# Optimization experiments

Hardware: AMD Instinct MI355X
Metric: run time of the kernel (lower is better)

The kernel has to match this reference:

```python
import jax, jax.numpy as jnp
import numpy as np

N_NODES = 100000   # nodes per node type
N_EDGES = 800000   # edges per edge type
F_IN = 128         # lazy (-1,-1) input feature dim, chosen == hidden
HID = 128          # hidden_channels
OUT = 1            # out_channels
N_LAYERS = 2
B = 256            # batch_size (num graphs)
NEG_SLOPE = 0.2    # GATConv default leaky_relu slope


def setup_inputs() -> dict:
    key = jax.random.key(0)
    ks = jax.random.split(key, 16)
    x_i = jax.random.normal(ks[0], (N_NODES, F_IN), jnp.float32)
    x_j = jax.random.normal(ks[1], (N_NODES, F_IN), jnp.float32)
    ei_ii = jax.random.randint(ks[2], (2, N_EDGES), 0, N_NODES, jnp.int32)
    ei_jj = jax.random.randint(ks[3], (2, N_EDGES), 0, N_NODES, jnp.int32)
    ei_ij = jax.random.randint(ks[4], (2, N_EDGES), 0, N_NODES, jnp.int32)
    ei_ji = jax.random.randint(ks[5], (2, N_EDGES), 0, N_NODES, jnp.int32)
    batch_i = jnp.sort(jax.random.randint(ks[6], (N_NODES,), 0, B, jnp.int32))
    batch_j = jnp.sort(jax.random.randint(ks[7], (N_NODES,), 0, B, jnp.int32))
    s = 1.0 / np.sqrt(HID)
    Ws = jax.random.normal(ks[8], (N_LAYERS, 4, F_IN, HID), jnp.float32) * s
    Wd = jax.random.normal(ks[9], (N_LAYERS, 4, F_IN, HID), jnp.float32) * s
    att_s = jax.random.normal(ks[10], (N_LAYERS, 4, HID), jnp.float32) * s
    att_d = jax.random.normal(ks[11], (N_LAYERS, 4, HID), jnp.float32) * s
    bias = jnp.zeros((N_LAYERS, 4, HID), jnp.float32)
    lin_w = jax.random.normal(ks[12], (HID, OUT), jnp.float32) * s
    lin_b = jnp.zeros((OUT,), jnp.float32)
    return dict(x_i=x_i, x_j=x_j, ei_ii=ei_ii, ei_jj=ei_jj, ei_ij=ei_ij,
                ei_ji=ei_ji, batch_i=batch_i, batch_j=batch_j, Ws=Ws, Wd=Wd,
                att_s=att_s, att_d=att_d, bias=bias, lin_w=lin_w, lin_b=lin_b)


def gat_conv(x_src, x_dst, edge, W_s, W_d, a_s, a_d, b):
    """Single-head GATConv: gather -> edge attention -> segment softmax -> scatter."""
    src, dst = edge[0], edge[1]
    n_dst = x_dst.shape[0]
    hs = x_src @ W_s                      # [Ns, C]
    hd = x_dst @ W_d                      # [Nd, C]
    e = jax.nn.leaky_relu((hs * a_s).sum(-1)[src] + (hd * a_d).sum(-1)[dst],
                          NEG_SLOPE)      # [E]
    m = jax.ops.segment_max(e, dst, num_segments=n_dst)
    m = jnp.where(jnp.isfinite(m), m, 0.0)  # empty segments -> 0
    p = jnp.exp(e - m[dst])
    denom = jax.ops.segment_sum(p, dst, num_segments=n_dst)
    alpha = p / jnp.maximum(denom[dst], 1e-16)
    out = jax.ops.segment_sum(alpha[:, None] * hs[src], dst, num_segments=n_dst)
    return out + b


def mean_pool(x, batch, size):
    s = jax.ops.segment_sum(x, batch, num_segments=size)
    cnt = jax.ops.segment_sum(jnp.ones((x.shape[0],), x.dtype), batch,
                              num_segments=size)
    return s / jnp.maximum(cnt, 1.0)[:, None]


def reference(x_i, x_j, ei_ii, ei_jj, ei_ij, ei_ji, batch_i, batch_j,
              Ws, Wd, att_s, att_d, bias, lin_w, lin_b):
    xi, xj = x_i, x_j
    for l in range(N_LAYERS):
        # edge-type order: 0=inner_i, 1=inner_j, 2=outer_ij, 3=outer_ji
        out_i = (gat_conv(xi, xi, ei_ii, Ws[l, 0], Wd[l, 0], att_s[l, 0], att_d[l, 0], bias[l, 0])
                 + gat_conv(xj, xi, ei_ji, Ws[l, 3], Wd[l, 3], att_s[l, 3], att_d[l, 3], bias[l, 3]))
        out_j = (gat_conv(xj, xj, ei_jj, Ws[l, 1], Wd[l, 1], att_s[l, 1], att_d[l, 1], bias[l, 1])
                 + gat_conv(xi, xj, ei_ij, Ws[l, 2], Wd[l, 2], att_s[l, 2], att_d[l, 2], bias[l, 2]))
        xi, xj = jnp.tanh(out_i), jnp.tanh(out_j)
    p_i = mean_pool(xi, batch_i, B)       # [B, HID]
    p_j = mean_pool(xj, batch_j, B)       # [B, HID]
    x = 0.5 * (p_i + p_j)                 # mean over the stacked pair
    return jax.nn.sigmoid(x @ lin_w + lin_b)
```

## Files before the change

### kernel.cpp

```cpp
#include <hip/hip_runtime.h>


#define NEG_SLOPE 0.2f

typedef __attribute__((ext_vector_type(8))) short short8v;
typedef __attribute__((ext_vector_type(4))) float float4v;

__device__ __forceinline__ unsigned short f2bf(float f) {
  unsigned u = __float_as_uint(f);
  unsigned r = (u + 0x7FFFu + ((u >> 16) & 1u)) >> 16;
  return (unsigned short)r;
}
__device__ __forceinline__ unsigned pack2(float a, float b) {
  return (unsigned)f2bf(a) | ((unsigned)f2bf(b) << 16);
}
__device__ __forceinline__ float bflo(unsigned u) {
  return __uint_as_float(u << 16);
}
__device__ __forceinline__ float bfhi(unsigned u) {
  return __uint_as_float(u & 0xFFFF0000u);
}
__device__ __forceinline__ float rl_f(float x, int lane) {
  return __int_as_float(__builtin_amdgcn_readlane(__float_as_int(x), lane));
}
__device__ __forceinline__ int rl_i(int x, int lane) {
  return __builtin_amdgcn_readlane(x, lane);
}

__global__ __launch_bounds__(256) void w_to_bf16t(const float* __restrict__ W,
                                                  unsigned short* __restrict__ Wt) {
  __shared__ float buf[64][129];
  int b = blockIdx.x, t = threadIdx.x;
  const float* w = W + (size_t)b * 16384;
  unsigned short* o = Wt + (size_t)b * 16384;
  for (int h = 0; h < 2; ++h) {
    for (int i = 0; i < 32; ++i) {
      int idx = i * 256 + t;
      buf[idx >> 7][idx & 127] = w[(size_t)(h * 64 + (idx >> 7)) * 128 + (idx & 127)];
    }
    __syncthreads();
    for (int i = 0; i < 32; ++i) {
      int idx = i * 256 + t;
      o[(size_t)(idx >> 6) * 128 + h * 64 + (idx & 63)] = f2bf(buf[idx & 63][idx >> 6]);
    }
    __syncthreads();
  }
}

__global__ void precompute_wa(const float* __restrict__ W,
                              const float* __restrict__ att,
                              float* __restrict__ out) {
  int idx = blockIdx.x;
  int f = threadIdx.x;
  const float* w = W + (size_t)idx * 128 * 128 + (size_t)f * 128;
  const float* a = att + idx * 128;
  float s = 0.f;
  #pragma unroll 8
  for (int h = 0; h < 128; ++h) s += w[h] * a[h];
  out[idx * 128 + f] = s;
}

template <int XBF16>
__global__ __launch_bounds__(256) void gemm_dual(
    const void* __restrict__ Xv,
    const unsigned short* __restrict__ Wt1, const float* __restrict__ att1,
    unsigned short* __restrict__ Hb1, float* __restrict__ as1,
    const unsigned short* __restrict__ Wt2, const float* __restrict__ att2,
    unsigned short* __restrict__ Hb2, float* __restrict__ as2,
    const float* __restrict__ vdA, const float* __restrict__ vdB,
    float* __restrict__ adA, float* __restrict__ adB, int M) {
  __shared__ unsigned short Xt[64][136];
  __shared__ unsigned short Wt[128][136];
  const int t = threadIdx.x;
  const int row0 = blockIdx.x * 64;

  {
    int r = t >> 2;
    int cq = (t & 3) * 32;
    int gr = row0 + r;
    if (gr >= M) gr = M - 1;
    if (XBF16) {
      const unsigned short* Xb = (const unsigned short*)Xv;
      const uint4* src = (const uint4*)(Xb + (size_t)gr * 128 + cq);
      #pragma unroll
      for (int i = 0; i < 4; ++i) *(uint4*)&Xt[r][cq + i * 8] = src[i];
    } else {
      const float* Xf = (const float*)Xv;
      const float4* src = (const float4*)(Xf + (size_t)gr * 128 + cq);
      #pragma unroll
      for (int i = 0; i < 8; ++i) {
        float4 v = src[i];
        uint2 u;
        u.x = pack2(v.x, v.y);
        u.y = pack2(v.z, v.w);
        *(uint2*)&Xt[r][cq + i * 4] = u;
      }
    }
  }
  {
    int n = t >> 1;
    int kh = (t & 1) * 64;
    const uint4* src = (const uint4*)(Wt1 + (size_t)n * 128 + kh);
    #pragma unroll
    for (int i = 0; i < 8; ++i) *(uint4*)&Wt[n][kh + i * 8] = src[i];
  }
  __syncthreads();

  if (t < 128) {
    int r = t & 63;
    const float* vd = (t < 64) ? vdA : vdB;
    float* adout = (t < 64) ? adA : adB;
    float sum = 0.f;
    #pragma unroll 4
    for (int k8 = 0; k8 < 16; ++k8) {
      uint4 u = *(const uint4*)&Xt[r][k8 * 8];
      const float* v = vd + k8 * 8;
      sum = fmaf(bflo(u.x), v[0], sum);
      sum = fmaf(bfhi(u.x), v[1], sum);
      sum = fmaf(bflo(u.y), v[2], sum);
      sum = fmaf(bfhi(u.y), v[3], sum);
      sum = fmaf(bflo(u.z), v[4], sum);
      sum = fmaf(bfhi(u.z), v[5], sum);
      sum = fmaf(bflo(u.w), v[6], sum);
      sum = fmaf(bfhi(u.w), v[7], sum);
    }
    int gr = row0 + r;
    if (gr < M) adout[gr] = sum;
  }

  const int lane = t & 63;
  const int wv = t >> 6;
  const int m = lane & 15;
  const int g = lane >> 4;
  const int ws = wv * 16;

  for (int ww = 0; ww < 2; ++ww) {
    if (ww == 1) {
      __syncthreads();
      int n = t >> 1;
      int kh = (t & 1) * 64;
      const uint4* src = (const uint4*)(Wt2 + (size_t)n * 128 + kh);
      #pragma unroll
      for (int i = 0; i < 8; ++i) *(uint4*)&Wt[n][kh + i * 8] = src[i];
      __syncthreads();
    }
    const float* att = ww ? att2 : att1;
    unsigned short* Hb = ww ? Hb2 : Hb1;
    float* as_ = ww ? as2 : as1;

    float4v acc[8];
    float4v z = {0.f, 0.f, 0.f, 0.f};
    #pragma unroll
    for (int nt = 0; nt < 8; ++nt) acc[nt] = z;

    #pragma unroll
    for (int ks = 0; ks < 4; ++ks) {
      short8v a = *(const short8v*)&Xt[ws + m][ks * 32 + g * 8];
      #pragma unroll
      for (int nt = 0; nt < 8; ++nt) {
        short8v b = *(const short8v*)&Wt[nt * 16 + m][ks * 32 + g * 8];
        acc[nt] = __builtin_amdgcn_mfma_f32_16x16x32_bf16(a, b, acc[nt], 0, 0, 0);
      }
    }

    {
      float attv[8];
      #pragma unroll
      for (int nt = 0; nt < 8; ++nt) attv[nt] = att[nt * 16 + m];
      #pragma unroll
      for (int r = 0; r < 4; ++r) {
        float s = 0.f;
        #pragma unroll
        for (int nt = 0; nt < 8; ++nt) s = fmaf(acc[nt][r], attv[nt], s);
        #pragma unroll
        for (int off = 1; off < 16; off <<= 1) s += __shfl_xor(s, off);
        if (m == 0) {
          int grow = row0 + ws + g * 4 + r;
          if (grow < M) as_[grow] = s;
        }
      }
    }

    #pragma unroll
    for (int nt = 0; nt < 8; ++nt) {
      #pragma unroll
      for (int r = 0; r < 4; ++r) {
        float v = acc[nt][r];
        float vn = __shfl_xor(v, 1);
        if ((m & 1) == 0) {
          int grow = row0 + ws + g * 4 + r;
          if (grow < M) {
            *(unsigned*)(Hb + (size_t)grow * 128 + nt * 16 + m) = pack2(v, vn);
          }
        }
      }
    }
  }
}

__global__ void hist4(const int* __restrict__ e0, const int* __restrict__ e1,
                      const int* __restrict__ e2, const int* __restrict__ e3,
                      int E, int* __restrict__ deg, int N) {
  int i = blockIdx.x * 256 + threadIdx.x;
  if (i >= E) return;
  int t = blockIdx.y;
  const int* ei = (t == 0) ? e0 : (t == 1) ? e1 : (t == 2) ? e2 : e3;
  atomicAdd(&deg[t * N + ei[E + i]], 1);
}

__global__ __launch_bounds__(1024) void scan4(const int* __restrict__ deg,
                                              int* __restrict__ rowptr, int N) {
  __shared__ int sums[1024];
  int t = threadIdx.x;
  int ty = blockIdx.x;
  const int* d = deg + (size_t)ty * N;
  int* rp = rowptr + (size_t)ty * (N + 1);
  int chunk = (N + 1023) / 1024;
  int lo = t * chunk;
  int hi = lo + chunk; if (hi > N) hi = N; if (lo > N) lo = N;
  int s = 0;
  for (int i = lo; i < hi; ++i) s += d[i];
  sums[t] = s;
  __syncthreads();
  for (int off = 1; off < 1024; off <<= 1) {
    int add = (t >= off) ? sums[t - off] : 0;
    __syncthreads();
    sums[t] += add;
    __syncthreads();
  }
  int run = (t == 0) ? 0 : sums[t - 1];
  for (int i = lo; i < hi; ++i) {
    rp[i] = run;
    run += d[i];
  }
  if (t == 1023) rp[N] = sums[1023];
}

__global__ void fill4(const int* __restrict__ e0, const int* __restrict__ e1,
                      const int* __restrict__ e2, const int* __restrict__ e3,
                      int E, const int* __restrict__ rowptr,
                      int* __restrict__ fill, int* __restrict__ csrc, int N) {
  int i = blockIdx.x * 256 + threadIdx.x;
  if (i >= E) return;
  int t = blockIdx.y;
  const int* ei = (t == 0) ? e0 : (t == 1) ? e1 : (t == 2) ? e2 : e3;
  int d = ei[E + i];
  int s = ei[i];
  int pos = rowptr[(size_t)t * (N + 1) + d] + atomicAdd(&fill[t * N + d], 1);
  csrc[(size_t)t * E + pos] = s;
}

__device__ __forceinline__ float2 agg_conv(const int* __restrict__ rowptr,
                                           const int* __restrict__ csrc,
                                           const unsigned short* __restrict__ hs,
                                           const float* __restrict__ as_,
                                           float ad, int n, int lane) {
  int beg = rowptr[n], end = rowptr[n + 1];
  float lsum = 0.f;
  float2 acc = make_float2(0.f, 0.f);
  for (int c = beg; c < end; c += 64) {
    int k = c + lane;
    bool valid = k < end;
    int s = valid ? csrc[k] : 0;
    float e = valid ? (as_[s] + ad) : 0.f;
    e = e > 0.f ? e : NEG_SLOPE * e;
    float p = valid ? __expf(e) : 0.f;
    float ps = p;
    #pragma unroll
    for (int off = 32; off >= 1; off >>= 1) ps += __shfl_xor(ps, off);
    lsum += ps;
    int cnt = end - c; if (cnt > 64) cnt = 64;
    for (int base = 0; base < cnt; base += 8) {
      float pk0 = rl_f(p, base + 0), pk1 = rl_f(p, base + 1);
      float pk2 = rl_f(p, base + 2), pk3 = rl_f(p, base + 3);
      float pk4 = rl_f(p, base + 4), pk5 = rl_f(p, base + 5);
      float pk6 = rl_f(p, base + 6), pk7 = rl_f(p, base + 7);
      int sk0 = rl_i(s, base + 0), sk1 = rl_i(s, base + 1);
      int sk2 = rl_i(s, base + 2), sk3 = rl_i(s, base + 3);
      int sk4 = rl_i(s, base + 4), sk5 = rl_i(s, base + 5);
      int sk6 = rl_i(s, base + 6), sk7 = rl_i(s, base + 7);
      unsigned u0 = *(const unsigned*)(hs + (size_t)sk0 * 128 + lane * 2);
      unsigned u1 = *(const unsigned*)(hs + (size_t)sk1 * 128 + lane * 2);
      unsigned u2 = *(const unsigned*)(hs + (size_t)sk2 * 128 + lane * 2);
      unsigned u3 = *(const unsigned*)(hs + (size_t)sk3 * 128 + lane * 2);
      unsigned u4 = *(const unsigned*)(hs + (size_t)sk4 * 128 + lane * 2);
      unsigned u5 = *(const unsigned*)(hs + (size_t)sk5 * 128 + lane * 2);
      unsigned u6 = *(const unsigned*)(hs + (size_t)sk6 * 128 + lane * 2);
      unsigned u7 = *(const unsigned*)(hs + (size_t)sk7 * 128 + lane * 2);
      acc.x = fmaf(pk0, bflo(u0), acc.x); acc.y = fmaf(pk0, bfhi(u0), acc.y);
      acc.x = fmaf(pk1, bflo(u1), acc.x); acc.y = fmaf(pk1, bfhi(u1), acc.y);
      acc.x = fmaf(pk2, bflo(u2), acc.x); acc.y = fmaf(pk2, bfhi(u2), acc.y);
      acc.x = fmaf(pk3, bflo(u3), acc.x); acc.y = fmaf(pk3, bfhi(u3), acc.y);
      acc.x = fmaf(pk4, bflo(u4), acc.x); acc.y = fmaf(pk4, bfhi(u4), acc.y);
      acc.x = fmaf(pk5, bflo(u5), acc.x); acc.y = fmaf(pk5, bfhi(u5), acc.y);
      acc.x = fmaf(pk6, bflo(u6), acc.x); acc.y = fmaf(pk6, bfhi(u6), acc.y);
      acc.x = fmaf(pk7, bflo(u7), acc.x); acc.y = fmaf(pk7, bfhi(u7), acc.y);
    }
  }
  float inv = 1.f / fmaxf(lsum, 1e-16f);
  acc.x *= inv;
  acc.y *= inv;
  return acc;
}

__global__ __launch_bounds__(256) void fused_agg_store(
    const int* __restrict__ rA, const int* __restrict__ sA,
    const unsigned short* __restrict__ hA, const float* __restrict__ asA,
    const float* __restrict__ adA, const int* __restrict__ rB,
    const int* __restrict__ sB, const unsigned short* __restrict__ hB,
    const float* __restrict__ asB, const float* __restrict__ adB,
    const float* __restrict__ biasA, const float* __restrict__ biasB,
    unsigned short* __restrict__ out, int N) {
  int wave = (blockIdx.x * 256 + threadIdx.x) >> 6;
  int lane = threadIdx.x & 63;
  if (wave >= N) return;
  float2 a = agg_conv(rA, sA, hA, asA, adA[wave], wave, lane);
  float2 b = agg_conv(rB, sB, hB, asB, adB[wave], wave, lane);
  float2 b1 = *(const float2*)(biasA + lane * 2);
  float2 b2 = *(const float2*)(biasB + lane * 2);
  float vx = tanhf(a.x + b.x + b1.x + b2.x);
  float vy = tanhf(a.y + b.y + b1.y + b2.y);
  *(unsigned*)(out + (size_t)wave * 128 + lane * 2) = pack2(vx, vy);
}

__global__ __launch_bounds__(256) void fused_agg_pool(
    const int* __restrict__ rA, const int* __restrict__ sA,
    const unsigned short* __restrict__ hA, const float* __restrict__ asA,
    const float* __restrict__ adA, const int* __restrict__ rB,
    const int* __restrict__ sB, const unsigned short* __restrict__ hB,
    const float* __restrict__ asB, const float* __restrict__ adB,
    const float* __restrict__ biasA, const float* __restrict__ biasB,
    const int* __restrict__ batch, float* __restrict__ pool, int N) {
  int wave = (blockIdx.x * 256 + threadIdx.x) >> 6;
  int lane = threadIdx.x & 63;
  if (wave >= N) return;
  float2 a = agg_conv(rA, sA, hA, asA, adA[wave], wave, lane);
  float2 b = agg_conv(rB, sB, hB, asB, adB[wave], wave, lane);
  float2 b1 = *(const float2*)(biasA + lane * 2);
  float2 b2 = *(const float2*)(biasB + lane * 2);
  float vx = tanhf(a.x + b.x + b1.x + b2.x);
  float vy = tanhf(a.y + b.y + b1.y + b2.y);
  int bb = batch[wave];
  float* p = pool + (size_t)bb * 128 + lane * 2;
  unsafeAtomicAdd(p, vx);
  unsafeAtomicAdd(p + 1, vy);
}

__device__ __forceinline__ int lower_bound_i(const int* __restrict__ a, int n,
                                             int v) {
  int lo = 0, hi = n;
  while (lo < hi) {
    int mid = (lo + hi) >> 1;
    if (a[mid] < v) lo = mid + 1; else hi = mid;
  }
  return lo;
}

__global__ void final_k(const float* __restrict__ pool_i,
                        const int* __restrict__ batch_i,
                        const float* __restrict__ pool_j,
                        const int* __restrict__ batch_j, int N,
                        const float* __restrict__ lin_w,
                        const float* __restrict__ lin_b,
                        float* __restrict__ out) {
  int b = threadIdx.x;
  float ci = (float)(lower_bound_i(batch_i, N, b + 1) -
                     lower_bound_i(batch_i, N, b));
  float cj = (float)(lower_bound_i(batch_j, N, b + 1) -
                     lower_bound_i(batch_j, N, b));
  ci = fmaxf(ci, 1.f);
  cj = fmaxf(cj, 1.f);
  float acc = 0.f;
  #pragma unroll 4
  for (int f = 0; f < 128; ++f) {
    float x = 0.5f * (pool_i[(size_t)b * 128 + f] / ci +
                      pool_j[(size_t)b * 128 + f] / cj);
    acc += x * lin_w[f];
  }
  acc += lin_b[0];
  out[b] = 1.f / (1.f + __expf(-acc));
}

extern "C" void kernel_launch(void* const* d_in, const int* in_sizes, int n_in,
                              void* d_out, int out_size, void* d_ws,
                              size_t ws_size, hipStream_t stream) {
  const float* x_i = (const float*)d_in[0];
  const float* x_j = (const float*)d_in[1];
  const int* ei_arr[4] = {(const int*)d_in[2], (const int*)d_in[3],
                          (const int*)d_in[4], (const int*)d_in[5]};
  const int* batch_i = (const int*)d_in[6];
  const int* batch_j = (const int*)d_in[7];
  const float* Ws = (const float*)d_in[8];
  const float* Wd = (const float*)d_in[9];
  const float* att_s = (const float*)d_in[10];
  const float* att_d = (const float*)d_in[11];
  const float* bias = (const float*)d_in[12];
  const float* lin_w = (const float*)d_in[13];
  const float* lin_b = (const float*)d_in[14];
  float* out = (float*)d_out;

  const int N = in_sizes[0] / 128;
  const int E = in_sizes[2] / 2;
  const size_t NF = (size_t)N * 128;

  char* w = (char*)d_ws;
  auto alloc = [&](size_t bytes) {
    char* p = w;
    w += (bytes + 255) & ~(size_t)255;
    return p;
  };
  unsigned short* bufA_i = (unsigned short*)alloc(NF * 2);
  unsigned short* bufA_j = (unsigned short*)alloc(NF * 2);
  unsigned short* hsb[4];
  for (int c = 0; c < 4; ++c) hsb[c] = (unsigned short*)alloc(NF * 2);
  int* csrc = (int*)alloc((size_t)4 * E * 4);
  int* rowptr = (int*)alloc((size_t)4 * (N + 1) * 4);
  int* deg = (int*)alloc((size_t)4 * N * 4);
  int* fillc = (int*)alloc((size_t)4 * N * 4);
  float* asb[4];
  for (int c = 0; c < 4; ++c) asb[c] = (float*)alloc((size_t)N * 4);
  float* adb[4];
  for (int c = 0; c < 4; ++c) adb[c] = (float*)alloc((size_t)N * 4);
  float* wdad = (float*)alloc(8 * 128 * 4);
  unsigned short* Wst = (unsigned short*)alloc(8 * 16384 * 2);
  float* pool = (float*)alloc(2 * 256 * 128 * 4);
  float* pool_i = pool;
  float* pool_j = pool + 256 * 128;

  w_to_bf16t<<<8, 256, 0, stream>>>(Ws, Wst);
  precompute_wa<<<8, 128, 0, stream>>>(Wd, att_d, wdad);

  hipMemsetAsync(deg, 0, (size_t)4 * N * 4, stream);
  hipMemsetAsync(fillc, 0, (size_t)4 * N * 4, stream);
  dim3 egrid((E + 255) / 256, 4);
  hist4<<<egrid, 256, 0, stream>>>(ei_arr[0], ei_arr[1], ei_arr[2], ei_arr[3],
                                   E, deg, N);
  scan4<<<4, 1024, 0, stream>>>(deg, rowptr, N);
  fill4<<<egrid, 256, 0, stream>>>(ei_arr[0], ei_arr[1], ei_arr[2], ei_arr[3],
                                   E, rowptr, fillc, csrc, N);

  hipMemsetAsync(pool, 0, 2 * 256 * 128 * 4, stream);

  const int gemm_blocks = (N + 63) / 64;
  const int nodew_blocks = (N + 3) / 4;

  for (int l = 0; l < 2; ++l) {
    const void* cur_i = (l == 0) ? (const void*)x_i : (const void*)bufA_i;
    const void* cur_j = (l == 0) ? (const void*)x_j : (const void*)bufA_j;
    const size_t L = (size_t)l * 4;

    if (l == 0) {
      gemm_dual<0><<<gemm_blocks, 256, 0, stream>>>(
          cur_i, Wst + (L + 0) * 16384, att_s + (L + 0) * 128, hsb[0], asb[0],
          Wst + (L + 2) * 16384, att_s + (L + 2) * 128, hsb[2], asb[2],
          wdad + (L + 0) * 128, wdad + (L + 3) * 128, adb[0], adb[3], N);
      gemm_dual<0><<<gemm_blocks, 256, 0, stream>>>(
          cur_j, Wst + (L + 1) * 16384, att_s + (L + 1) * 128, hsb[1], asb[1],
          Wst + (L + 3) * 16384, att_s + (L + 3) * 128, hsb[3], asb[3],
          wdad + (L + 1) * 128, wdad + (L + 2) * 128, adb[1], adb[2], N);
    } else {
      gemm_dual<1><<<gemm_blocks, 256, 0, stream>>>(
          cur_i, Wst + (L + 0) * 16384, att_s + (L + 0) * 128, hsb[0], asb[0],
          Wst + (L + 2) * 16384, att_s + (L + 2) * 128, hsb[2], asb[2],
          wdad + (L + 0) * 128, wdad + (L + 3) * 128, adb[0], adb[3], N);
      gemm_dual<1><<<gemm_blocks, 256, 0, stream>>>(
          cur_j, Wst + (L + 1) * 16384, att_s + (L + 1) * 128, hsb[1], asb[1],
          Wst + (L + 3) * 16384, att_s + (L + 3) * 128, hsb[3], asb[3],
          wdad + (L + 1) * 128, wdad + (L + 2) * 128, adb[1], adb[2], N);
    }

    for (int pair = 0; pair < 2; ++pair) {
      int cA = (pair == 0) ? 0 : 1;
      int cB = (pair == 0) ? 3 : 2;
      const int* rA = rowptr + (size_t)cA * (N + 1);
      const int* rB = rowptr + (size_t)cB * (N + 1);
      const int* sA = csrc + (size_t)cA * E;
      const int* sB = csrc + (size_t)cB * E;
      const float* bA = bias + (L + cA) * 128;
      const float* bB = bias + (L + cB) * 128;
      if (l == 0) {
        unsigned short* outb = (pair == 0) ? bufA_i : bufA_j;
        fused_agg_store<<<nodew_blocks, 256, 0, stream>>>(
            rA, sA, hsb[cA], asb[cA], adb[cA], rB, sB, hsb[cB], asb[cB],
            adb[cB], bA, bB, outb, N);
      } else {
        const int* batch = (pair == 0) ? batch_i : batch_j;
        float* poolp = (pair == 0) ? pool_i : pool_j;
        fused_agg_pool<<<nodew_blocks, 256, 0, stream>>>(
            rA, sA, hsb[cA], asb[cA], adb[cA], rB, sB, hsb[cB], asb[cB],
            adb[cB], bA, bB, batch, poolp, N);
      }
    }
  }

  final_k<<<1, 256, 0, stream>>>(pool_i, batch_i, pool_j, batch_j, N, lin_w,
                                 lin_b, out);
}
```

Before: 1.179 ms.

## Interleave both edge types' gathers per node and merge pair launches into one grid

The per-node aggregation now walks both incoming edge types in the same loop, issuing 16 independent feature-row gathers per step instead of 8, to expose more memory-level parallelism. The softmax denominator is accumulated from readlane values rather than a separate wave shuffle reduction. The two per-destination-type launches are merged into a single 2D grid, which removes a launch and the tail between them. In exchange, register pressure rises and when degrees differ the loop runs to the larger of the two counts, with some lanes doing masked work.

```diff
diff --git a/kernel.cpp b/kernel.cpp
--- a/kernel.cpp
+++ b/kernel.cpp
@@ -250,94 +250,129 @@
   csrc[(size_t)t * E + pos] = s;
 }
 
-__device__ __forceinline__ float2 agg_conv(const int* __restrict__ rowptr,
-                                           const int* __restrict__ csrc,
-                                           const unsigned short* __restrict__ hs,
-                                           const float* __restrict__ as_,
-                                           float ad, int n, int lane) {
-  int beg = rowptr[n], end = rowptr[n + 1];
-  float lsum = 0.f;
-  float2 acc = make_float2(0.f, 0.f);
-  for (int c = beg; c < end; c += 64) {
-    int k = c + lane;
-    bool valid = k < end;
-    int s = valid ? csrc[k] : 0;
-    float e = valid ? (as_[s] + ad) : 0.f;
-    e = e > 0.f ? e : NEG_SLOPE * e;
-    float p = valid ? __expf(e) : 0.f;
-    float ps = p;
-    #pragma unroll
-    for (int off = 32; off >= 1; off >>= 1) ps += __shfl_xor(ps, off);
-    lsum += ps;
-    int cnt = end - c; if (cnt > 64) cnt = 64;
+struct PairArgs {
+  const int* rA; const int* sA; const unsigned short* hA;
+  const float* asA; const float* adA;
+  const int* rB; const int* sB; const unsigned short* hB;
+  const float* asB; const float* adB;
+  const float* biasA; const float* biasB;
+};
+
+__device__ __forceinline__ void agg_pair(const PairArgs& P, int n, int lane,
+                                         float2& outA, float2& outB) {
+  int begA = P.rA[n], endA = P.rA[n + 1];
+  int begB = P.rB[n], endB = P.rB[n + 1];
+  float adA = P.adA[n], adB = P.adB[n];
+  float lsA = 0.f, lsB = 0.f;
+  float2 aA = make_float2(0.f, 0.f), aB = make_float2(0.f, 0.f);
+  int cA = begA, cB = begB;
+  while (cA < endA || cB < endB) {
+    int kA = cA + lane, kB = cB + lane;
+    bool vA = kA < endA;
+    bool vB = kB < endB;
+    int sA = vA ? P.sA[kA] : 0;
+    int sB = vB ? P.sB[kB] : 0;
+    float eA = vA ? (P.asA[sA] + adA) : 0.f;
+    float eB = vB ? (P.asB[sB] + adB) : 0.f;
+    eA = eA > 0.f ? eA : NEG_SLOPE * eA;
+    eB = eB > 0.f ? eB : NEG_SLOPE * eB;
+    float pA = vA ? __expf(eA) : 0.f;
+    float pB = vB ? __expf(eB) : 0.f;
+    int cntA = endA - cA; cntA = cntA < 0 ? 0 : (cntA > 64 ? 64 : cntA);
+    int cntB = endB - cB; cntB = cntB < 0 ? 0 : (cntB > 64 ? 64 : cntB);
+    int cnt = cntA > cntB ? cntA : cntB;
     for (int base = 0; base < cnt; base += 8) {
-      float pk0 = rl_f(p, base + 0), pk1 = rl_f(p, base + 1);
-      float pk2 = rl_f(p, base + 2), pk3 = rl_f(p, base + 3);
-      float pk4 = rl_f(p, base + 4), pk5 = rl_f(p, base + 5);
-      float pk6 = rl_f(p, base + 6), pk7 = rl_f(p, base + 7);
-      int sk0 = rl_i(s, base + 0), sk1 = rl_i(s, base + 1);
-      int sk2 = rl_i(s, base + 2), sk3 = rl_i(s, base + 3);
-      int sk4 = rl_i(s, base + 4), sk5 = rl_i(s, base + 5);
-      int sk6 = rl_i(s, base + 6), sk7 = rl_i(s, base + 7);
-      unsigned u0 = *(const unsigned*)(hs + (size_t)sk0 * 128 + lane * 2);
-      unsigned u1 = *(const unsigned*)(hs + (size_t)sk1 * 128 + lane * 2);
-      unsigned u2 = *(const unsigned*)(hs + (size_t)sk2 * 128 + lane * 2);
-      unsigned u3 = *(const unsigned*)(hs + (size_t)sk3 * 128 + lane * 2);
-      unsigned u4 = *(const unsigned*)(hs + (size_t)sk4 * 128 + lane * 2);
-      unsigned u5 = *(const unsigned*)(hs + (size_t)sk5 * 128 + lane * 2);
-      unsigned u6 = *(const unsigned*)(hs + (size_t)sk6 * 128 + lane * 2);
-      unsigned u7 = *(const unsigned*)(hs + (size_t)sk7 * 128 + lane * 2);
-      acc.x = fmaf(pk0, bflo(u0), acc.x); acc.y = fmaf(pk0, bfhi(u0), acc.y);
-      acc.x = fmaf(pk1, bflo(u1), acc.x); acc.y = fmaf(pk1, bfhi(u1), acc.y);
-      acc.x = fmaf(pk2, bflo(u2), acc.x); acc.y = fmaf(pk2, bfhi(u2), acc.y);
-      acc.x = fmaf(pk3, bflo(u3), acc.x); acc.y = fmaf(pk3, bfhi(u3), acc.y);
-      acc.x = fmaf(pk4, bflo(u4), acc.x); acc.y = fmaf(pk4, bfhi(u4), acc.y);
-      acc.x = fmaf(pk5, bflo(u5), acc.x); acc.y = fmaf(pk5, bfhi(u5), acc.y);
-      acc.x = fmaf(pk6, bflo(u6), acc.x); acc.y = fmaf(pk6, bfhi(u6), acc.y);
-      acc.x = fmaf(pk7, bflo(u7), acc.x); acc.y = fmaf(pk7, bfhi(u7), acc.y);
-    }
-  }
-  float inv = 1.f / fmaxf(lsum, 1e-16f);
-  acc.x *= inv;
-  acc.y *= inv;
-  return acc;
-}
-
-__global__ __launch_bounds__(256) void fused_agg_store(
-    const int* __restrict__ rA, const int* __restrict__ sA,
-    const unsigned short* __restrict__ hA, const float* __restrict__ asA,
-    const float* __restrict__ adA, const int* __restrict__ rB,
-    const int* __restrict__ sB, const unsigned short* __restrict__ hB,
-    const float* __restrict__ asB, const float* __restrict__ adB,
-    const float* __restrict__ biasA, const float* __restrict__ biasB,
-    unsigned short* __restrict__ out, int N) {
+      float qa0 = rl_f(pA, base + 0), qa1 = rl_f(pA, base + 1);
+      float qa2 = rl_f(pA, base + 2), qa3 = rl_f(pA, base + 3);
+      float qa4 = rl_f(pA, base + 4), qa5 = rl_f(pA, base + 5);
+      float qa6 = rl_f(pA, base + 6), qa7 = rl_f(pA, base + 7);
+      float qb0 = rl_f(pB, base + 0), qb1 = rl_f(pB, base + 1);
+      float qb2 = rl_f(pB, base + 2), qb3 = rl_f(pB, base + 3);
+      float qb4 = rl_f(pB, base + 4), qb5 = rl_f(pB, base + 5);
+      float qb6 = rl_f(pB, base + 6), qb7 = rl_f(pB, base + 7);
+      int ta0 = rl_i(sA, base + 0), ta1 = rl_i(sA, base + 1);
+      int ta2 = rl_i(sA, base + 2), ta3 = rl_i(sA, base + 3);
+      int ta4 = rl_i(sA, base + 4), ta5 = rl_i(sA, base + 5);
+      int ta6 = rl_i(sA, base + 6), ta7 = rl_i(sA, base + 7);
+      int tb0 = rl_i(sB, base + 0), tb1 = rl_i(sB, base + 1);
+      int tb2 = rl_i(sB, base + 2), tb3 = rl_i(sB, base + 3);
+      int tb4 = rl_i(sB, base + 4), tb5 = rl_i(sB, base + 5);
+      int tb6 = rl_i(sB, base + 6), tb7 = rl_i(sB, base + 7);
+      unsigned ua0 = *(const unsigned*)(P.hA + (size_t)ta0 * 128 + lane * 2);
+      unsigned ua1 = *(const unsigned*)(P.hA + (size_t)ta1 * 128 + lane * 2);
+      unsigned ua2 = *(const unsigned*)(P.hA + (size_t)ta2 * 128 + lane * 2);
+      unsigned ua3 = *(const unsigned*)(P.hA + (size_t)ta3 * 128 + lane * 2);
+      unsigned ua4 = *(const unsigned*)(P.hA + (size_t)ta4 * 128 + lane * 2);
+      unsigned ua5 = *(const unsigned*)(P.hA + (size_t)ta5 * 128 + lane * 2);
+      unsigned ua6 = *(const unsigned*)(P.hA + (size_t)ta6 * 128 + lane * 2);
+      unsigned ua7 = *(const unsigned*)(P.hA + (size_t)ta7 * 128 + lane * 2);
+      unsigned ub0 = *(const unsigned*)(P.hB + (size_t)tb0 * 128 + lane * 2);
+      unsigned ub1 = *(const unsigned*)(P.hB + (size_t)tb1 * 128 + lane * 2);
+      unsigned ub2 = *(const unsigned*)(P.hB + (size_t)tb2 * 128 + lane * 2);
+      unsigned ub3 = *(const unsigned*)(P.hB + (size_t)tb3 * 128 + lane * 2);
+      unsigned ub4 = *(const unsigned*)(P.hB + (size_t)tb4 * 128 + lane * 2);
+      unsigned ub5 = *(const unsigned*)(P.hB + (size_t)tb5 * 128 + lane * 2);
+      unsigned ub6 = *(const unsigned*)(P.hB + (size_t)tb6 * 128 + lane * 2);
+      unsigned ub7 = *(const unsigned*)(P.hB + (size_t)tb7 * 128 + lane * 2);
+      lsA += ((qa0 + qa1) + (qa2 + qa3)) + ((qa4 + qa5) + (qa6 + qa7));
+      lsB += ((qb0 + qb1) + (qb2 + qb3)) + ((qb4 + qb5) + (qb6 + qb7));
+      aA.x = fmaf(qa0, bflo(ua0), aA.x); aA.y = fmaf(qa0, bfhi(ua0), aA.y);
+      aA.x = fmaf(qa1, bflo(ua1), aA.x); aA.y = fmaf(qa1, bfhi(ua1), aA.y);
+      aA.x = fmaf(qa2, bflo(ua2), aA.x); aA.y = fmaf(qa2, bfhi(ua2), aA.y);
+      aA.x = fmaf(qa3, bflo(ua3), aA.x); aA.y = fmaf(qa3, bfhi(ua3), aA.y);
+      aA.x = fmaf(qa4, bflo(ua4), aA.x); aA.y = fmaf(qa4, bfhi(ua4), aA.y);
+      aA.x = fmaf(qa5, bflo(ua5), aA.x); aA.y = fmaf(qa5, bfhi(ua5), aA.y);
+      aA.x = fmaf(qa6, bflo(ua6), aA.x); aA.y = fmaf(qa6, bfhi(ua6), aA.y);
+      aA.x = fmaf(qa7, bflo(ua7), aA.x); aA.y = fmaf(qa7, bfhi(ua7), aA.y);
+      aB.x = fmaf(qb0, bflo(ub0), aB.x); aB.y = fmaf(qb0, bfhi(ub0), aB.y);
+      aB.x = fmaf(qb1, bflo(ub1), aB.x); aB.y = fmaf(qb1, bfhi(ub1), aB.y);
+      aB.x = fmaf(qb2, bflo(ub2), aB.x); aB.y = fmaf(qb2, bfhi(ub2), aB.y);
+      aB.x = fmaf(qb3, bflo(ub3), aB.x); aB.y = fmaf(qb3, bfhi(ub3), aB.y);
+      aB.x = fmaf(qb4, bflo(ub4), aB.x); aB.y = fmaf(qb4, bfhi(ub4), aB.y);
+      aB.x = fmaf(qb5, bflo(ub5), aB.x); aB.y = fmaf(qb5, bfhi(ub5), aB.y);
+      aB.x = fmaf(qb6, bflo(ub6), aB.x); aB.y = fmaf(qb6, bfhi(ub6), aB.y);
+      aB.x = fmaf(qb7, bflo(ub7), aB.x); aB.y = fmaf(qb7, bfhi(ub7), aB.y);
+    }
+    cA += 64;
+    cB += 64;
+  }
+  float invA = 1.f / fmaxf(lsA, 1e-16f);
+  float invB = 1.f / fmaxf(lsB, 1e-16f);
+  outA = make_float2(aA.x * invA, aA.y * invA);
+  outB = make_float2(aB.x * invB, aB.y * invB);
+}
+
+__global__ __launch_bounds__(256) void agg_store2(
+    PairArgs P0, unsigned short* __restrict__ out0,
+    PairArgs P1, unsigned short* __restrict__ out1, int N) {
   int wave = (blockIdx.x * 256 + threadIdx.x) >> 6;
   int lane = threadIdx.x & 63;
   if (wave >= N) return;
-  float2 a = agg_conv(rA, sA, hA, asA, adA[wave], wave, lane);
-  float2 b = agg_conv(rB, sB, hB, asB, adB[wave], wave, lane);
-  float2 b1 = *(const float2*)(biasA + lane * 2);
-  float2 b2 = *(const float2*)(biasB + lane * 2);
+  const PairArgs& P = blockIdx.y ? P1 : P0;
+  unsigned short* out = blockIdx.y ? out1 : out0;
+  float2 a, b;
+  agg_pair(P, wave, lane, a, b);
+  float2 b1 = *(const float2*)(P.biasA + lane * 2);
+  float2 b2 = *(const float2*)(P.biasB + lane * 2);
   float vx = tanhf(a.x + b.x + b1.x + b2.x);
   float vy = tanhf(a.y + b.y + b1.y + b2.y);
   *(unsigned*)(out + (size_t)wave * 128 + lane * 2) = pack2(vx, vy);
 }
 
-__global__ __launch_bounds__(256) void fused_agg_pool(
-    const int* __restrict__ rA, const int* __restrict__ sA,
-    const unsigned short* __restrict__ hA, const float* __restrict__ asA,
-    const float* __restrict__ adA, const int* __restrict__ rB,
-    const int* __restrict__ sB, const unsigned short* __restrict__ hB,
-    const float* __restrict__ asB, const float* __restrict__ adB,
-    const float* __restrict__ biasA, const float* __restrict__ biasB,
-    const int* __restrict__ batch, float* __restrict__ pool, int N) {
+__global__ __launch_bounds__(256) void agg_pool2(
+    PairArgs P0, const int* __restrict__ batch0, float* __restrict__ pool0,
+    PairArgs P1, const int* __restrict__ batch1, float* __restrict__ pool1,
+    int N) {
   int wave = (blockIdx.x * 256 + threadIdx.x) >> 6;
   int lane = threadIdx.x & 63;
   if (wave >= N) return;
-  float2 a = agg_conv(rA, sA, hA, asA, adA[wave], wave, lane);
-  float2 b = agg_conv(rB, sB, hB, asB, adB[wave], wave, lane);
-  float2 b1 = *(const float2*)(biasA + lane * 2);
-  float2 b2 = *(const float2*)(biasB + lane * 2);
+  const PairArgs& P = blockIdx.y ? P1 : P0;
+  const int* batch = blockIdx.y ? batch1 : batch0;
+  float* pool = blockIdx.y ? pool1 : pool0;
+  float2 a, b;
+  agg_pair(P, wave, lane, a, b);
+  float2 b1 = *(const float2*)(P.biasA + lane * 2);
+  float2 b2 = *(const float2*)(P.biasB + lane * 2);
   float vx = tanhf(a.x + b.x + b1.x + b2.x);
   float vy = tanhf(a.y + b.y + b1.y + b2.y);
   int bb = batch[wave];
@@ -469,27 +504,23 @@
           wdad + (L + 1) * 128, wdad + (L + 2) * 128, adb[1], adb[2], N);
     }
 
-    for (int pair = 0; pair < 2; ++pair) {
-      int cA = (pair == 0) ? 0 : 1;
-      int cB = (pair == 0) ? 3 : 2;
-      const int* rA = rowptr + (size_t)cA * (N + 1);
-      const int* rB = rowptr + (size_t)cB * (N + 1);
-      const int* sA = csrc + (size_t)cA * E;
-      const int* sB = csrc + (size_t)cB * E;
-      const float* bA = bias + (L + cA) * 128;
-      const float* bB = bias + (L + cB) * 128;
-      if (l == 0) {
-        unsigned short* outb = (pair == 0) ? bufA_i : bufA_j;
-        fused_agg_store<<<nodew_blocks, 256, 0, stream>>>(
-            rA, sA, hsb[cA], asb[cA], adb[cA], rB, sB, hsb[cB], asb[cB],
-            adb[cB], bA, bB, outb, N);
-      } else {
-        const int* batch = (pair == 0) ? batch_i : batch_j;
-        float* poolp = (pair == 0) ? pool_i : pool_j;
-        fused_agg_pool<<<nodew_blocks, 256, 0, stream>>>(
-            rA, sA, hsb[cA], asb[cA], adb[cA], rB, sB, hsb[cB], asb[cB],
-            adb[cB], bA, bB, batch, poolp, N);
-      }
+    PairArgs P0 = {rowptr + (size_t)0 * (N + 1), csrc + (size_t)0 * E, hsb[0],
+                   asb[0], adb[0],
+                   rowptr + (size_t)3 * (N + 1), csrc + (size_t)3 * E, hsb[3],
+                   asb[3], adb[3],
+                   bias + (L + 0) * 128, bias + (L + 3) * 128};
+    PairArgs P1 = {rowptr + (size_t)1 * (N + 1), csrc + (size_t)1 * E, hsb[1],
+                   asb[1], adb[1],
+                   rowptr + (size_t)2 * (N + 1), csrc + (size_t)2 * E, hsb[2],
+                   asb[2], adb[2],
+                   bias + (L + 1) * 128, bias + (L + 2) * 128};
+
+    dim3 agrid(nodew_blocks, 2);
+    if (l == 0) {
+      agg_store2<<<agrid, 256, 0, stream>>>(P0, bufA_i, P1, bufA_j, N);
+    } else {
+      agg_pool2<<<agrid, 256, 0, stream>>>(P0, batch_i, pool_i, P1, batch_j,
+                                           pool_j, N);
     }
   }
 
```

New measurement: 1.109 ms. 5.9% less time.
